# Kernel optimization log

Hardware: AMD Instinct MI355X
Metric: run time of the kernel (lower is better)

## Reference

```python
import jax, jax.numpy as jnp
import numpy as np

LN_EPS = 1e-5

def setup_inputs() -> dict:
    key = jax.random.key(0)
    ks = jax.random.split(key, 4)
    B, D, H, K = 8192, 4096, 2048, 512
    return {
        "x": jax.random.normal(ks[0], (B, D), jnp.float32),
        "beta": jax.random.normal(ks[1], (D, K), jnp.float32) * 0.01,
        "compound_mean": jnp.zeros((D,), jnp.float32),
        "W1": jax.random.normal(ks[2], (H, D), jnp.float32) * 0.02,
        "b1": jnp.zeros((H,), jnp.float32),
        "ln_w": jnp.ones((H,), jnp.float32),
        "ln_b": jnp.zeros((H,), jnp.float32),
        "W2": jax.random.normal(ks[3], (K, H), jnp.float32) * 0.02,
        "b2": jnp.zeros((K,), jnp.float32),
    }

def reference(x, beta, compound_mean, W1, b1, ln_w, ln_b, W2, b2):
    # compound path of BiQBMVAE.forward (compound=True)
    h = jnp.einsum('bd,hd->bh', x - compound_mean, W1) + b1      # fc1
    mu = jnp.mean(h, axis=-1, keepdims=True)                      # LayerNorm
    var = jnp.mean(jnp.square(h - mu), axis=-1, keepdims=True)
    h = (h - mu) * jax.lax.rsqrt(var + LN_EPS) * ln_w + ln_b
    h = jax.nn.relu(h)                                            # act_fn
    q_logits = jnp.einsum('bh,kh->bk', h, W2) + b2                # fc2 -> [B, k]
    x_recon = jax.nn.sigmoid(jnp.einsum('bk,dk->bd', q_logits, beta))  # decode_compound
    return (q_logits, x_recon, q_logits, q_logits)
```

## Files before the change

kernel.cpp:

```cpp
#include <hip/hip_runtime.h>
#include <hip/hip_bf16.h>
#include <cstddef>
#include <cstdint>

#define LN_EPS 1e-5f

#define B_DIM 8192
#define D_DIM 4096
#define H_DIM 2048
#define K_DIM 512

typedef __bf16 bf16x8_t __attribute__((ext_vector_type(8)));
typedef float f32x4_t __attribute__((ext_vector_type(4)));

__device__ __forceinline__ void gl2lds16(const __hip_bfloat16* g,
                                         __hip_bfloat16* l) {
  __builtin_amdgcn_global_load_lds(
      (const __attribute__((address_space(1))) uint32_t*)g,
      (__attribute__((address_space(3))) uint32_t*)l, 16, 0, 0);
}

__global__ __launch_bounds__(256) void conv_all_kernel(
    const float* __restrict__ x, const float* __restrict__ cmean,
    __hip_bfloat16* __restrict__ xb, const float* __restrict__ W1,
    const float* __restrict__ W2, const float* __restrict__ beta,
    __hip_bfloat16* __restrict__ W1b, __hip_bfloat16* __restrict__ W2b,
    __hip_bfloat16* __restrict__ betab) {
  const int blk = blockIdx.x;
  if (blk < 16384) {
    const long i = (((long)blk << 8) + threadIdx.x) << 3;
    const int col = (int)(i & (D_DIM - 1));
    const float4 a = *(const float4*)(x + i);
    const float4 b = *(const float4*)(x + i + 4);
    const float4 ma = *(const float4*)(cmean + col);
    const float4 mb = *(const float4*)(cmean + col + 4);
    union { __hip_bfloat16 h[8]; uint4 u; } pk;
    pk.h[0] = __float2bfloat16(a.x - ma.x);
    pk.h[1] = __float2bfloat16(a.y - ma.y);
    pk.h[2] = __float2bfloat16(a.z - ma.z);
    pk.h[3] = __float2bfloat16(a.w - ma.w);
    pk.h[4] = __float2bfloat16(b.x - mb.x);
    pk.h[5] = __float2bfloat16(b.y - mb.y);
    pk.h[6] = __float2bfloat16(b.z - mb.z);
    pk.h[7] = __float2bfloat16(b.w - mb.w);
    *(uint4*)(xb + i) = pk.u;
    return;
  }
  const int b2 = blk - 16384;
  const float* src;
  __hip_bfloat16* dst;
  long base;
  if (b2 < 4096) {
    src = W1; dst = W1b; base = b2;
  } else if (b2 < 4608) {
    src = W2; dst = W2b; base = b2 - 4096;
  } else {
    src = beta; dst = betab; base = b2 - 4608;
  }
  const long i = ((base << 8) + threadIdx.x) << 3;
  const float4 a = *(const float4*)(src + i);
  const float4 b = *(const float4*)(src + i + 4);
  union { __hip_bfloat16 h[8]; uint4 u; } pk;
  pk.h[0] = __float2bfloat16(a.x);
  pk.h[1] = __float2bfloat16(a.y);
  pk.h[2] = __float2bfloat16(a.z);
  pk.h[3] = __float2bfloat16(a.w);
  pk.h[4] = __float2bfloat16(b.x);
  pk.h[5] = __float2bfloat16(b.y);
  pk.h[6] = __float2bfloat16(b.z);
  pk.h[7] = __float2bfloat16(b.w);
  *(uint4*)(dst + i) = pk.u;
}

template <int EPI>
__global__ __launch_bounds__(512, 2) void gemm256_bg(
    const __hip_bfloat16* __restrict__ A, int lda,
    const __hip_bfloat16* __restrict__ Bm, int ldb,
    const float* __restrict__ bias, float* __restrict__ C0, int ldc, int Kd) {
  constexpr int SLOT = 8192;
  __shared__ __hip_bfloat16 lds[4 * SLOT];

  const int t_ = threadIdx.x;
  const int lane = t_ & 63;
  const int wv = t_ >> 6;
  const int wr = wv >> 2;
  const int wc = wv & 3;
  const int fr = lane & 15;
  const int ko = lane >> 4;
  const int kos = (ko ^ ((fr >> 1) & 3)) * 8;

  const int gx = gridDim.x;
  const int nwg = gx * gridDim.y;
  const int f = blockIdx.y * gx + blockIdx.x;
  const int w = (f & 7) * (nwg >> 3) + (f >> 3);
  const int bx = w % gx;
  const int by = w / gx;

  const long rowA = (long)by * 256;
  const long rowB = (long)bx * 256;

  const int ci = (wv << 6) + lane;
  const int srow = ci >> 2;
  const int skq = (ci & 3) ^ ((ci >> 3) & 3);
  const __hip_bfloat16* sA0 = A + (rowA + srow) * (long)lda + skq * 8;
  const __hip_bfloat16* sA1 = sA0 + 128L * lda;

  auto STG = [&](int s, int k0) {
    __hip_bfloat16* d = lds + s * SLOT + wv * 512;
    gl2lds16(sA0 + k0, d);
    gl2lds16(sA1 + k0, d + 4096);
  };

  const __hip_bfloat16* pB = Bm + (rowB + wc * 64 + fr) * (long)ldb + ko * 8;
  const long bStep = 16L * ldb;

  f32x4_t acc[8][4];
  const f32x4_t zero = {0.f, 0.f, 0.f, 0.f};
#pragma unroll
  for (int a = 0; a < 8; ++a)
#pragma unroll
    for (int b = 0; b < 4; ++b) acc[a][b] = zero;

  const int NT = Kd >> 5;

  bf16x8_t cb[4], nb[4];
#pragma unroll
  for (int ni = 0; ni < 4; ++ni)
    cb[ni] = *(const bf16x8_t*)(pB + ni * bStep);
  STG(0, 0);
  STG(1, 32);
  STG(2, 64);
  asm volatile("s_waitcnt vmcnt(2)" ::: "memory");
  __builtin_amdgcn_s_barrier();
  __builtin_amdgcn_sched_barrier(0);

  bf16x8_t F0a[4], F1a[4];
#pragma unroll
  for (int mi = 0; mi < 4; ++mi)
    F0a[mi] = *(const bf16x8_t*)&lds[(wr * 128 + mi * 16 + fr) * 32 + kos];

  auto BODY = [&](int t, bf16x8_t(&cf)[4], bf16x8_t(&cbv)[4],
                  bf16x8_t(&nf)[4], bf16x8_t(&nbv)[4]) {
    const int st = (t & 3) * SLOT;
    const bool pfA = (t + 3) < NT;
    const bool pfB = (t + 1) < NT;
    if (pfA) STG((t + 3) & 3, (t + 3) * 32);
    if (pfB) {
      const int kk = (t + 1) * 32;
#pragma unroll
      for (int ni = 0; ni < 4; ++ni)
        nbv[ni] = *(const bf16x8_t*)(pB + ni * bStep + kk);
    }
    bf16x8_t ag[4];
#pragma unroll
    for (int mi = 0; mi < 4; ++mi)
      ag[mi] =
          *(const bf16x8_t*)&lds[st + (wr * 128 + 64 + mi * 16 + fr) * 32 +
                                 kos];
    if (pfB) {
      const int s1 = ((t + 1) & 3) * SLOT;
#pragma unroll
      for (int mi = 0; mi < 4; ++mi)
        nf[mi] =
            *(const bf16x8_t*)&lds[s1 + (wr * 128 + mi * 16 + fr) * 32 + kos];
    }
    __builtin_amdgcn_s_setprio(1);
#pragma unroll
    for (int mi = 0; mi < 4; ++mi)
#pragma unroll
      for (int ni = 0; ni < 4; ++ni)
        acc[mi][ni] = __builtin_amdgcn_mfma_f32_16x16x32_bf16(
            cf[mi], cbv[ni], acc[mi][ni], 0, 0, 0);
#pragma unroll
    for (int mi = 0; mi < 4; ++mi)
#pragma unroll
      for (int ni = 0; ni < 4; ++ni)
        acc[4 + mi][ni] = __builtin_amdgcn_mfma_f32_16x16x32_bf16(
            ag[mi], cbv[ni], acc[4 + mi][ni], 0, 0, 0);
    __builtin_amdgcn_s_setprio(0);
    if (pfB) {
      if (pfA)
        asm volatile("s_waitcnt vmcnt(6)" ::: "memory");
      else
        asm volatile("s_waitcnt vmcnt(4)" ::: "memory");
      __builtin_amdgcn_s_barrier();
      __builtin_amdgcn_sched_barrier(0);
    }
  };

  for (int t = 0; t < NT; t += 2) {
    BODY(t, F0a, cb, F1a, nb);
    BODY(t + 1, F1a, nb, F0a, cb);
  }

  const long cRow0 = rowA + wr * 128;
  const int cCol0 = (int)rowB + wc * 64;
#pragma unroll
  for (int a = 0; a < 8; ++a) {
#pragma unroll
    for (int b = 0; b < 4; ++b) {
      f32x4_t v4 = acc[a][b];
      const int col = cCol0 + b * 16 + fr;
#pragma unroll
      for (int r = 0; r < 4; ++r) {
        const long row = cRow0 + a * 16 + ko * 4 + r;
        float val = v4[r];
        if constexpr (EPI == 0) {
          val += bias[col];
        } else {
          val = 1.f / (1.f + __expf(-val));
        }
        C0[row * (long)ldc + col] = val;
      }
    }
  }
}

template <int EPI>
__global__ __launch_bounds__(512, 4) void gemm128_ring(
    const __hip_bfloat16* __restrict__ A, int lda,
    const __hip_bfloat16* __restrict__ Bm, int ldb,
    const float* __restrict__ bias, float* __restrict__ C0, int ldc,
    float* __restrict__ C2, float* __restrict__ C3,
    __hip_bfloat16* __restrict__ Cb, int Kd) {
  constexpr int SLOT = 8192;
  __shared__ __hip_bfloat16 lds[4 * SLOT];

  const int t_ = threadIdx.x;
  const int lane = t_ & 63;
  const int wv = t_ >> 6;
  const int wr = wv >> 2;
  const int wc = wv & 3;
  const int fr = lane & 15;
  const int ko = lane >> 4;
  const int kos = (ko ^ ((fr >> 1) & 3)) * 8;

  const int gx = gridDim.x;
  const int nwg = gx * gridDim.y;
  const int f = blockIdx.y * gx + blockIdx.x;
  const int w = (f & 7) * (nwg >> 3) + (f >> 3);
  const int bx = w % gx;
  const int by = w / gx;

  const long rowA = (long)by * 128;
  const long rowB = (long)bx * 128;

  const int ci = (wv << 6) + lane;
  const int srow = ci >> 2;
  const int skq = (ci & 3) ^ ((ci >> 3) & 3);
  const __hip_bfloat16* sA = A + (rowA + srow) * (long)lda + skq * 8;
  const __hip_bfloat16* sB = Bm + (rowB + srow) * (long)ldb + skq * 8;

  auto STG = [&](int s, int k0) {
    __hip_bfloat16* d = lds + s * SLOT + wv * 512;
    gl2lds16(sA + k0, d);
    gl2lds16(sB + k0, d + 4096);
  };

  f32x4_t acc[4][2];
  const f32x4_t zero = {0.f, 0.f, 0.f, 0.f};
#pragma unroll
  for (int a = 0; a < 4; ++a)
#pragma unroll
    for (int b = 0; b < 2; ++b) acc[a][b] = zero;

  const int NT = Kd >> 5;

  STG(0, 0);
  STG(1, 32);
  STG(2, 64);
  asm volatile("s_waitcnt vmcnt(2)" ::: "memory");
  __builtin_amdgcn_s_barrier();
  __builtin_amdgcn_sched_barrier(0);

  bf16x8_t F0a[4], F0b[2], F1a[4], F1b[2];
#pragma unroll
  for (int mi = 0; mi < 4; ++mi)
    F0a[mi] = *(const bf16x8_t*)&lds[(wr * 64 + mi * 16 + fr) * 32 + kos];
#pragma unroll
  for (int ni = 0; ni < 2; ++ni)
    F0b[ni] =
        *(const bf16x8_t*)&lds[4096 + (wc * 32 + ni * 16 + fr) * 32 + kos];

  auto BODY = [&](int t, bf16x8_t(&cf)[4], bf16x8_t(&cb)[2],
                  bf16x8_t(&nf)[4], bf16x8_t(&nb)[2]) {
    if (t + 3 < NT) STG((t + 3) & 3, (t + 3) * 32);
    if (t + 1 < NT) {
      const int s1 = ((t + 1) & 3) * SLOT;
#pragma unroll
      for (int mi = 0; mi < 4; ++mi)
        nf[mi] =
            *(const bf16x8_t*)&lds[s1 + (wr * 64 + mi * 16 + fr) * 32 + kos];
#pragma unroll
      for (int ni = 0; ni < 2; ++ni)
        nb[ni] = *(const bf16x8_t*)&lds[s1 + 4096 +
                                        (wc * 32 + ni * 16 + fr) * 32 + kos];
    }
    __builtin_amdgcn_s_setprio(1);
#pragma unroll
    for (int mi = 0; mi < 4; ++mi)
#pragma unroll
      for (int ni = 0; ni < 2; ++ni)
        acc[mi][ni] = __builtin_amdgcn_mfma_f32_16x16x32_bf16(
            cf[mi], cb[ni], acc[mi][ni], 0, 0, 0);
    __builtin_amdgcn_s_setprio(0);
    if (t + 1 < NT) {
      if (t + 3 < NT)
        asm volatile("s_waitcnt vmcnt(2)" ::: "memory");
      else
        asm volatile("s_waitcnt vmcnt(0)" ::: "memory");
      __builtin_amdgcn_s_barrier();
      __builtin_amdgcn_sched_barrier(0);
    }
  };

  for (int t = 0; t < NT; t += 2) {
    BODY(t, F0a, F0b, F1a, F1b);
    BODY(t + 1, F1a, F1b, F0a, F0b);
  }

  const long cRow0 = rowA + wr * 64;
  const int cCol0 = (int)rowB + wc * 32;
#pragma unroll
  for (int a = 0; a < 4; ++a) {
#pragma unroll
    for (int b = 0; b < 2; ++b) {
      f32x4_t v4 = acc[a][b];
      const int col = cCol0 + b * 16 + fr;
#pragma unroll
      for (int r = 0; r < 4; ++r) {
        const long row = cRow0 + a * 16 + ko * 4 + r;
        float val = v4[r];
        if constexpr (EPI == 1) {
          val += bias[col];
          C0[row * (long)ldc + col] = val;
          C2[row * (long)ldc + col] = val;
          C3[row * (long)ldc + col] = val;
          Cb[row * (long)ldc + col] = __float2bfloat16(val);
        } else {
          val = 1.f / (1.f + __expf(-val));
          C0[row * (long)ldc + col] = val;
        }
      }
    }
  }
}

__global__ __launch_bounds__(256) void ln_relu_kernel(
    void* hptr, const float* __restrict__ ln_w, const float* __restrict__ ln_b) {
  const int H = H_DIM;
  float* h = (float*)hptr;
  __hip_bfloat16* hb = (__hip_bfloat16*)hptr;

  const long row = blockIdx.x;
  const int t = threadIdx.x;
  const int lane = t & 63;
  const int wv = t >> 6;
  const float* hr = h + row * H + t * 8;

  const float4 va = *(const float4*)hr;
  const float4 vb = *(const float4*)(hr + 4);
  float v[8] = {va.x, va.y, va.z, va.w, vb.x, vb.y, vb.z, vb.w};

  __shared__ float red[8];

  float s = 0.f;
#pragma unroll
  for (int i = 0; i < 8; ++i) s += v[i];
#pragma unroll
  for (int off = 32; off; off >>= 1) s += __shfl_down(s, off);
  if (lane == 0) red[wv] = s;
  __syncthreads();
  const float mu = (red[0] + red[1] + red[2] + red[3]) * (1.f / (float)H);

  float vs = 0.f;
#pragma unroll
  for (int i = 0; i < 8; ++i) {
    float d = v[i] - mu;
    vs += d * d;
  }
#pragma unroll
  for (int off = 32; off; off >>= 1) vs += __shfl_down(vs, off);
  if (lane == 0) red[4 + wv] = vs;
  __syncthreads();
  const float var = (red[4] + red[5] + red[6] + red[7]) * (1.f / (float)H);
  const float rs = rsqrtf(var + LN_EPS);

  const float4 wa = *(const float4*)(ln_w + t * 8);
  const float4 wb = *(const float4*)(ln_w + t * 8 + 4);
  const float4 ba = *(const float4*)(ln_b + t * 8);
  const float4 bb = *(const float4*)(ln_b + t * 8 + 4);
  const float wgt[8] = {wa.x, wa.y, wa.z, wa.w, wb.x, wb.y, wb.z, wb.w};
  const float bia[8] = {ba.x, ba.y, ba.z, ba.w, bb.x, bb.y, bb.z, bb.w};

  union { __hip_bfloat16 hh[8]; uint4 u; } pk;
#pragma unroll
  for (int i = 0; i < 8; ++i) {
    float y = (v[i] - mu) * rs * wgt[i] + bia[i];
    pk.hh[i] = __float2bfloat16(fmaxf(y, 0.f));
  }
  *(uint4*)(hb + row * (long)D_DIM + t * 8) = pk.u;
}

extern "C" void kernel_launch(void* const* d_in, const int* in_sizes, int n_in,
                              void* d_out, int out_size, void* d_ws,
                              size_t ws_size, hipStream_t stream) {
  const float* x = (const float*)d_in[0];
  const float* beta = (const float*)d_in[1];
  const float* cmean = (const float*)d_in[2];
  const float* W1 = (const float*)d_in[3];
  const float* b1 = (const float*)d_in[4];
  const float* ln_w = (const float*)d_in[5];
  const float* ln_b = (const float*)d_in[6];
  const float* W2 = (const float*)d_in[7];
  const float* b2 = (const float*)d_in[8];

  float* out = (float*)d_out;
  float* q0 = out;
  float* xr = out + (size_t)B_DIM * K_DIM;
  float* q2 = xr + (size_t)B_DIM * D_DIM;
  float* q3 = q2 + (size_t)B_DIM * K_DIM;

  __hip_bfloat16* xb = (__hip_bfloat16*)xr;
  float* h = xr + (size_t)B_DIM * D_DIM / 2;
  __hip_bfloat16* hb = (__hip_bfloat16*)h;

  __hip_bfloat16* W1b = (__hip_bfloat16*)d_ws;
  __hip_bfloat16* W2b = W1b + (size_t)H_DIM * D_DIM;
  __hip_bfloat16* betab = W2b + (size_t)K_DIM * H_DIM;
  __hip_bfloat16* qb = betab + (size_t)D_DIM * K_DIM;

  dim3 blk(256, 1, 1);
  dim3 blk512(512, 1, 1);

  hipLaunchKernelGGL(conv_all_kernel, dim3(16384 + 4096 + 512 + 1024), blk, 0,
                     stream, x, cmean, xb, W1, W2, beta, W1b, W2b, betab);

  hipLaunchKernelGGL((gemm256_bg<0>), dim3(H_DIM / 256, B_DIM / 256), blk512,
                     0, stream, xb, D_DIM, W1b, D_DIM, b1, h, H_DIM, D_DIM);

  hipLaunchKernelGGL(ln_relu_kernel, dim3(B_DIM), blk, 0, stream, (void*)h,
                     ln_w, ln_b);

  hipLaunchKernelGGL((gemm128_ring<1>), dim3(K_DIM / 128, B_DIM / 128),
                     blk512, 0, stream, hb, D_DIM, W2b, H_DIM, b2, q0, K_DIM,
                     q2, q3, qb, H_DIM);

  hipLaunchKernelGGL((gemm128_ring<2>), dim3(D_DIM / 128, B_DIM / 128),
                     blk512, 0, stream, qb, K_DIM, betab, K_DIM,
                     (const float*)nullptr, xr, D_DIM, (float*)nullptr,
                     (float*)nullptr, (__hip_bfloat16*)nullptr, K_DIM);
}
```

Measured before the change: 590.2 us.

## Stage B operand through LDS ring in 256 GEMM and add branchless scheduled main loop

The fc1 GEMM now loads both A and B tiles into a 4-slot LDS ring via global_load_lds, instead of reading B fragments directly from global memory into registers. Both GEMM kernels gain a branch-free main-loop body for steady state, with sched_group_barrier hints to interleave VMEM, LDS reads and MFMA. The aim is to hide B global-load latency and cut per-iteration branching. Doubling the LDS slot to 128KB per block likely limits occupancy to one block per CU, which conflicts with the launch bound of 2.

```diff
diff --git a/kernel.cpp b/kernel.cpp
--- a/kernel.cpp
+++ b/kernel.cpp
@@ -12,6 +12,11 @@
 
 typedef __bf16 bf16x8_t __attribute__((ext_vector_type(8)));
 typedef float f32x4_t __attribute__((ext_vector_type(4)));
+
+#define SGB __builtin_amdgcn_sched_group_barrier
+#define SG_MFMA 0x008
+#define SG_VMEM 0x070
+#define SG_DSRD 0x100
 
 __device__ __forceinline__ void gl2lds16(const __hip_bfloat16* g,
                                          __hip_bfloat16* l) {
@@ -73,11 +78,11 @@
 }
 
 template <int EPI>
-__global__ __launch_bounds__(512, 2) void gemm256_bg(
+__global__ __launch_bounds__(512, 2) void gemm256_ring(
     const __hip_bfloat16* __restrict__ A, int lda,
     const __hip_bfloat16* __restrict__ Bm, int ldb,
     const float* __restrict__ bias, float* __restrict__ C0, int ldc, int Kd) {
-  constexpr int SLOT = 8192;
+  constexpr int SLOT = 16384;
   __shared__ __hip_bfloat16 lds[4 * SLOT];
 
   const int t_ = threadIdx.x;
@@ -104,15 +109,16 @@
   const int skq = (ci & 3) ^ ((ci >> 3) & 3);
   const __hip_bfloat16* sA0 = A + (rowA + srow) * (long)lda + skq * 8;
   const __hip_bfloat16* sA1 = sA0 + 128L * lda;
+  const __hip_bfloat16* sB0 = Bm + (rowB + srow) * (long)ldb + skq * 8;
+  const __hip_bfloat16* sB1 = sB0 + 128L * ldb;
 
   auto STG = [&](int s, int k0) {
     __hip_bfloat16* d = lds + s * SLOT + wv * 512;
     gl2lds16(sA0 + k0, d);
     gl2lds16(sA1 + k0, d + 4096);
+    gl2lds16(sB0 + k0, d + 8192);
+    gl2lds16(sB1 + k0, d + 12288);
   };
-
-  const __hip_bfloat16* pB = Bm + (rowB + wc * 64 + fr) * (long)ldb + ko * 8;
-  const long bStep = 16L * ldb;
 
   f32x4_t acc[8][4];
   const f32x4_t zero = {0.f, 0.f, 0.f, 0.f};
@@ -123,46 +129,83 @@
 
   const int NT = Kd >> 5;
 
-  bf16x8_t cb[4], nb[4];
-#pragma unroll
-  for (int ni = 0; ni < 4; ++ni)
-    cb[ni] = *(const bf16x8_t*)(pB + ni * bStep);
   STG(0, 0);
   STG(1, 32);
   STG(2, 64);
-  asm volatile("s_waitcnt vmcnt(2)" ::: "memory");
+  asm volatile("s_waitcnt vmcnt(4)" ::: "memory");
   __builtin_amdgcn_s_barrier();
   __builtin_amdgcn_sched_barrier(0);
 
-  bf16x8_t F0a[4], F1a[4];
+  bf16x8_t F0a[4], F0b[4], F1a[4], F1b[4];
 #pragma unroll
   for (int mi = 0; mi < 4; ++mi)
     F0a[mi] = *(const bf16x8_t*)&lds[(wr * 128 + mi * 16 + fr) * 32 + kos];
-
-  auto BODY = [&](int t, bf16x8_t(&cf)[4], bf16x8_t(&cbv)[4],
-                  bf16x8_t(&nf)[4], bf16x8_t(&nbv)[4]) {
+#pragma unroll
+  for (int ni = 0; ni < 4; ++ni)
+    F0b[ni] =
+        *(const bf16x8_t*)&lds[8192 + (wc * 64 + ni * 16 + fr) * 32 + kos];
+
+  auto BODY_MAIN = [&](int t, bf16x8_t(&cf)[4], bf16x8_t(&cb)[4],
+                       bf16x8_t(&nf)[4], bf16x8_t(&nb)[4]) {
     const int st = (t & 3) * SLOT;
-    const bool pfA = (t + 3) < NT;
-    const bool pfB = (t + 1) < NT;
-    if (pfA) STG((t + 3) & 3, (t + 3) * 32);
-    if (pfB) {
-      const int kk = (t + 1) * 32;
-#pragma unroll
-      for (int ni = 0; ni < 4; ++ni)
-        nbv[ni] = *(const bf16x8_t*)(pB + ni * bStep + kk);
-    }
+    const int s1 = ((t + 1) & 3) * SLOT;
+    STG((t + 3) & 3, (t + 3) * 32);
     bf16x8_t ag[4];
 #pragma unroll
     for (int mi = 0; mi < 4; ++mi)
       ag[mi] =
           *(const bf16x8_t*)&lds[st + (wr * 128 + 64 + mi * 16 + fr) * 32 +
                                  kos];
-    if (pfB) {
+#pragma unroll
+    for (int mi = 0; mi < 4; ++mi)
+      nf[mi] =
+          *(const bf16x8_t*)&lds[s1 + (wr * 128 + mi * 16 + fr) * 32 + kos];
+#pragma unroll
+    for (int ni = 0; ni < 4; ++ni)
+      nb[ni] = *(const bf16x8_t*)&lds[s1 + 8192 +
+                                      (wc * 64 + ni * 16 + fr) * 32 + kos];
+    __builtin_amdgcn_s_setprio(1);
+#pragma unroll
+    for (int mi = 0; mi < 4; ++mi)
+#pragma unroll
+      for (int ni = 0; ni < 4; ++ni)
+        acc[mi][ni] = __builtin_amdgcn_mfma_f32_16x16x32_bf16(
+            cf[mi], cb[ni], acc[mi][ni], 0, 0, 0);
+#pragma unroll
+    for (int mi = 0; mi < 4; ++mi)
+#pragma unroll
+      for (int ni = 0; ni < 4; ++ni)
+        acc[4 + mi][ni] = __builtin_amdgcn_mfma_f32_16x16x32_bf16(
+            ag[mi], cb[ni], acc[4 + mi][ni], 0, 0, 0);
+    __builtin_amdgcn_s_setprio(0);
+    SGB(SG_VMEM, 4, 0);
+    SGB(SG_DSRD, 12, 0);
+    SGB(SG_MFMA, 32, 0);
+    asm volatile("s_waitcnt vmcnt(4)" ::: "memory");
+    __builtin_amdgcn_s_barrier();
+    __builtin_amdgcn_sched_barrier(0);
+  };
+
+  auto BODY = [&](int t, bf16x8_t(&cf)[4], bf16x8_t(&cb)[4],
+                  bf16x8_t(&nf)[4], bf16x8_t(&nb)[4]) {
+    const int st = (t & 3) * SLOT;
+    if (t + 3 < NT) STG((t + 3) & 3, (t + 3) * 32);
+    bf16x8_t ag[4];
+#pragma unroll
+    for (int mi = 0; mi < 4; ++mi)
+      ag[mi] =
+          *(const bf16x8_t*)&lds[st + (wr * 128 + 64 + mi * 16 + fr) * 32 +
+                                 kos];
+    if (t + 1 < NT) {
       const int s1 = ((t + 1) & 3) * SLOT;
 #pragma unroll
       for (int mi = 0; mi < 4; ++mi)
         nf[mi] =
             *(const bf16x8_t*)&lds[s1 + (wr * 128 + mi * 16 + fr) * 32 + kos];
+#pragma unroll
+      for (int ni = 0; ni < 4; ++ni)
+        nb[ni] = *(const bf16x8_t*)&lds[s1 + 8192 +
+                                        (wc * 64 + ni * 16 + fr) * 32 + kos];
     }
     __builtin_amdgcn_s_setprio(1);
 #pragma unroll
@@ -170,27 +213,32 @@
 #pragma unroll
       for (int ni = 0; ni < 4; ++ni)
         acc[mi][ni] = __builtin_amdgcn_mfma_f32_16x16x32_bf16(
-            cf[mi], cbv[ni], acc[mi][ni], 0, 0, 0);
+            cf[mi], cb[ni], acc[mi][ni], 0, 0, 0);
 #pragma unroll
     for (int mi = 0; mi < 4; ++mi)
 #pragma unroll
       for (int ni = 0; ni < 4; ++ni)
         acc[4 + mi][ni] = __builtin_amdgcn_mfma_f32_16x16x32_bf16(
-            ag[mi], cbv[ni], acc[4 + mi][ni], 0, 0, 0);
+            ag[mi], cb[ni], acc[4 + mi][ni], 0, 0, 0);
     __builtin_amdgcn_s_setprio(0);
-    if (pfB) {
-      if (pfA)
-        asm volatile("s_waitcnt vmcnt(6)" ::: "memory");
+    if (t + 1 < NT) {
+      if (t + 3 < NT)
+        asm volatile("s_waitcnt vmcnt(4)" ::: "memory");
       else
-        asm volatile("s_waitcnt vmcnt(4)" ::: "memory");
+        asm volatile("s_waitcnt vmcnt(0)" ::: "memory");
       __builtin_amdgcn_s_barrier();
       __builtin_amdgcn_sched_barrier(0);
     }
   };
 
-  for (int t = 0; t < NT; t += 2) {
-    BODY(t, F0a, cb, F1a, nb);
-    BODY(t + 1, F1a, nb, F0a, cb);
+  int t = 0;
+  for (; t + 4 < NT; t += 2) {
+    BODY_MAIN(t, F0a, F0b, F1a, F1b);
+    BODY_MAIN(t + 1, F1a, F1b, F0a, F0b);
+  }
+  for (; t < NT; t += 2) {
+    BODY(t, F0a, F0b, F1a, F1b);
+    BODY(t + 1, F1a, F1b, F0a, F0b);
   }
 
   const long cRow0 = rowA + wr * 128;
@@ -281,6 +329,34 @@
   for (int ni = 0; ni < 2; ++ni)
     F0b[ni] =
         *(const bf16x8_t*)&lds[4096 + (wc * 32 + ni * 16 + fr) * 32 + kos];
+
+  auto BODY_MAIN = [&](int t, bf16x8_t(&cf)[4], bf16x8_t(&cb)[2],
+                       bf16x8_t(&nf)[4], bf16x8_t(&nb)[2]) {
+    const int s1 = ((t + 1) & 3) * SLOT;
+    STG((t + 3) & 3, (t + 3) * 32);
+#pragma unroll
+    for (int mi = 0; mi < 4; ++mi)
+      nf[mi] =
+          *(const bf16x8_t*)&lds[s1 + (wr * 64 + mi * 16 + fr) * 32 + kos];
+#pragma unroll
+    for (int ni = 0; ni < 2; ++ni)
+      nb[ni] = *(const bf16x8_t*)&lds[s1 + 4096 +
+                                      (wc * 32 + ni * 16 + fr) * 32 + kos];
+    __builtin_amdgcn_s_setprio(1);
+#pragma unroll
+    for (int mi = 0; mi < 4; ++mi)
+#pragma unroll
+      for (int ni = 0; ni < 2; ++ni)
+        acc[mi][ni] = __builtin_amdgcn_mfma_f32_16x16x32_bf16(
+            cf[mi], cb[ni], acc[mi][ni], 0, 0, 0);
+    __builtin_amdgcn_s_setprio(0);
+    SGB(SG_VMEM, 2, 0);
+    SGB(SG_DSRD, 6, 0);
+    SGB(SG_MFMA, 8, 0);
+    asm volatile("s_waitcnt vmcnt(2)" ::: "memory");
+    __builtin_amdgcn_s_barrier();
+    __builtin_amdgcn_sched_barrier(0);
+  };
 
   auto BODY = [&](int t, bf16x8_t(&cf)[4], bf16x8_t(&cb)[2],
                   bf16x8_t(&nf)[4], bf16x8_t(&nb)[2]) {
@@ -314,7 +390,12 @@
     }
   };
 
-  for (int t = 0; t < NT; t += 2) {
+  int t = 0;
+  for (; t + 4 < NT; t += 2) {
+    BODY_MAIN(t, F0a, F0b, F1a, F1b);
+    BODY_MAIN(t + 1, F1a, F1b, F0a, F0b);
+  }
+  for (; t < NT; t += 2) {
     BODY(t, F0a, F0b, F1a, F1b);
     BODY(t + 1, F1a, F1b, F0a, F0b);
   }
@@ -436,8 +517,9 @@
   hipLaunchKernelGGL(conv_all_kernel, dim3(16384 + 4096 + 512 + 1024), blk, 0,
                      stream, x, cmean, xb, W1, W2, beta, W1b, W2b, betab);
 
-  hipLaunchKernelGGL((gemm256_bg<0>), dim3(H_DIM / 256, B_DIM / 256), blk512,
-                     0, stream, xb, D_DIM, W1b, D_DIM, b1, h, H_DIM, D_DIM);
+  hipLaunchKernelGGL((gemm256_ring<0>), dim3(H_DIM / 256, B_DIM / 256),
+                     blk512, 0, stream, xb, D_DIM, W1b, D_DIM, b1, h, H_DIM,
+                     D_DIM);
 
   hipLaunchKernelGGL(ln_relu_kernel, dim3(B_DIM), blk, 0, stream, (void*)h,
                      ln_w, ln_b);
```

Measured after the change: 519.8 us. 11.9% less time.
